# Optimization experiments

Measured on AMD Instinct MI355X. Metric: run time of the kernel, lower is better.

The kernel has to match this reference:

```python
import jax, jax.numpy as jnp
import numpy as np

N, E, D, H, G, C = 50000, 800000, 128, 128, 256, 10
BN_EPS = 1e-5

def _lin_init(key, fan_in, fan_out):
    k1, k2 = jax.random.split(key)
    bound = 1.0 / np.sqrt(fan_in)
    w = jax.random.uniform(k1, (fan_in, fan_out), jnp.float32, -bound, bound)
    b = jax.random.uniform(k2, (fan_out,), jnp.float32, -bound, bound)
    return w, b

def setup_inputs() -> dict:
    key = jax.random.key(0)
    ks = jax.random.split(key, 16)
    x = jax.random.normal(ks[0], (N, D), jnp.float32)
    edge_index = jax.random.randint(ks[1], (2, E), 0, N, jnp.int64)
    batch = jnp.sort(jax.random.randint(ks[2], (N,), 0, G, jnp.int64))
    inp = {"x": x, "edge_index": edge_index, "batch": batch}
    # per-layer GIN MLP params: Linear-ReLU-Linear-ReLU-BN
    dims = [(D, H), (H, H), (H, H)]
    for i, (din, dh) in enumerate(dims, start=1):
        wa, ba = _lin_init(ks[2 + 2 * i], din, dh)
        wb, bb = _lin_init(ks[3 + 2 * i], dh, dh)
        inp[f"w{i}a"], inp[f"b{i}a"] = wa, ba
        inp[f"w{i}b"], inp[f"b{i}b"] = wb, bb
        inp[f"g{i}"] = jnp.ones((dh,), jnp.float32)
        inp[f"bt{i}"] = jnp.zeros((dh,), jnp.float32)
    inp["eps"] = jnp.zeros((3,), jnp.float32)  # train_eps=True, init 0
    inp["lw1"], inp["lb1"] = _lin_init(ks[10], H, H)
    inp["lw2"], inp["lb2"] = _lin_init(ks[11], H, C)
    return inp

def _gin_layer(x, src, dst, eps_i, wa, ba, wb, bb, g, bt):
    # scatter-add neighbor aggregation: out[i] = sum_{j->i} x[j]
    agg = jax.ops.segment_sum(x[src], dst, num_segments=N)
    h = (1.0 + eps_i) * x + agg
    h = jax.nn.relu(h @ wa + ba)
    h = jax.nn.relu(h @ wb + bb)
    mu = h.mean(axis=0)
    var = ((h - mu) ** 2).mean(axis=0)  # biased var (torch BN normalization)
    return g * (h - mu) * jax.lax.rsqrt(var + BN_EPS) + bt

def reference(x, edge_index, batch, w1a, b1a, w1b, b1b, g1, bt1,
              w2a, b2a, w2b, b2b, g2, bt2, w3a, b3a, w3b, b3b, g3, bt3,
              eps, lw1, lb1, lw2, lb2):
    src, dst = edge_index[0], edge_index[1]
    h = _gin_layer(x, src, dst, eps[0], w1a, b1a, w1b, b1b, g1, bt1)
    h = _gin_layer(h, src, dst, eps[1], w2a, b2a, w2b, b2b, g2, bt2)
    h = _gin_layer(h, src, dst, eps[2], w3a, b3a, w3b, b3b, g3, bt3)
    # global mean pool over batch ids
    sums = jax.ops.segment_sum(h, batch, num_segments=G)
    cnt = jax.ops.segment_sum(jnp.ones((N,), h.dtype), batch, num_segments=G)
    pooled = sums / jnp.maximum(cnt, 1.0)[:, None]
    z = jax.nn.relu(pooled @ lw1 + lb1)
    # dropout omitted (eval / deterministic reference)
    z = z @ lw2 + lb2
    return jax.nn.log_softmax(z, axis=-1)
```

## Files before the change

### kernel.cpp

```cpp
#include <hip/hip_runtime.h>

#define N_NODES 50000
#define N_EDGES 800000
#define DIM 128
#define N_GRAPHS 256
#define N_CLS 10
#define BN_EPSV 1e-5f
#define CAP 64
#define RSIZE 6250
#define NBLK ((N_NODES + 63) / 64)

typedef __attribute__((ext_vector_type(8))) short short8;
typedef __attribute__((ext_vector_type(4))) float f32x4;

__device__ __forceinline__ float bf2f(short u) {
  return __uint_as_float(((unsigned)(unsigned short)u) << 16);
}
__device__ __forceinline__ unsigned short f2bf(float f) {
  unsigned u = __float_as_uint(f);
  unsigned r = (u + 0x7FFFu + ((u >> 16) & 1u)) >> 16;
  return (unsigned short)r;
}
__device__ __forceinline__ int swz(int row, int bytecol) {
  return row * 256 + (bytecol ^ ((row & 7) << 4));
}


__global__ void cvt_x_kernel(const float* __restrict__ x, ushort* __restrict__ xb) {
  int i = blockIdx.x * blockDim.x + threadIdx.x;
  int stride = gridDim.x * blockDim.x;
  const int tot = N_NODES * DIM / 4;
  for (; i < tot; i += stride) {
    float4 v = ((const float4*)x)[i];
    ushort4 o;
    o.x = f2bf(v.x); o.y = f2bf(v.y); o.z = f2bf(v.z); o.w = f2bf(v.w);
    ((ushort4*)xb)[i] = o;
  }
}

__global__ void cvt_w_kernel(const float* __restrict__ w0, const float* __restrict__ w1,
                             const float* __restrict__ w2, const float* __restrict__ w3,
                             const float* __restrict__ w4, const float* __restrict__ w5,
                             ushort* __restrict__ wt) {
  int m = blockIdx.x >> 6;
  const float* w = m == 0 ? w0 : m == 1 ? w1 : m == 2 ? w2 : m == 3 ? w3
                                                       : m == 4 ? w4 : w5;
  int idx = (blockIdx.x & 63) * 256 + threadIdx.x;
  int k = idx >> 7, n = idx & 127;
  wt[m * 16384 + n * 128 + k] = f2bf(w[idx]);
}


__global__ __launch_bounds__(256) void fill_kernel(
    const int* __restrict__ src, const int* __restrict__ dst,
    int* __restrict__ cnt, ushort* __restrict__ csr) {
  int cls = blockIdx.x & 7;
  int lo = cls * RSIZE;
  int hi = lo + RSIZE;
  int i = (blockIdx.x >> 3) * blockDim.x + threadIdx.x;
  int stride = (gridDim.x >> 3) * blockDim.x;
  for (; i < N_EDGES; i += stride) {
    int d = dst[i];
    if (d >= lo && d < hi) {
      int p = atomicAdd(&cnt[d], 1);
      if (p < CAP) csr[(size_t)d * CAP + p] = (ushort)src[i];
    }
  }
}


template <bool FIRST>
__global__ __launch_bounds__(256, 8) void gather_kernel(
    const ushort* __restrict__ xin, const int* __restrict__ cnt,
    const ushort* __restrict__ csr, const float* __restrict__ pstats,
    const float* __restrict__ pgamma, const float* __restrict__ pbeta,
    const float* __restrict__ epsp, int layer, ushort* __restrict__ agg) {
  int node = (blockIdx.x * blockDim.x + threadIdx.x) >> 6;
  if (node >= N_NODES) return;
  int l = threadIdx.x & 63;
  int li = l & 15, lg = l >> 4;
  float epv = 1.0f + epsp[layer];
  int deg = cnt[node];
  deg = deg < CAP ? deg : CAP;
  const ushort* nb = csr + (size_t)node * CAP;
  float av[8];
#pragma unroll
  for (int j = 0; j < 8; j++) av[j] = 0.f;
  if (lg == 0) {
    short8 sv = *(const short8*)(xin + (size_t)node * DIM + li * 8);
#pragma unroll
    for (int j = 0; j < 8; j++) av[j] = epv * bf2f(sv[j]);
  }
  int i = lg;
  for (; i + 12 < deg; i += 16) {
    int j0 = nb[i], j1 = nb[i + 4], j2 = nb[i + 8], j3 = nb[i + 12];
    short8 v0 = *(const short8*)(xin + (size_t)j0 * DIM + li * 8);
    short8 v1 = *(const short8*)(xin + (size_t)j1 * DIM + li * 8);
    short8 v2 = *(const short8*)(xin + (size_t)j2 * DIM + li * 8);
    short8 v3 = *(const short8*)(xin + (size_t)j3 * DIM + li * 8);
#pragma unroll
    for (int j = 0; j < 8; j++)
      av[j] += (bf2f(v0[j]) + bf2f(v1[j])) + (bf2f(v2[j]) + bf2f(v3[j]));
  }
  for (; i < deg; i += 4) {
    int j0 = nb[i];
    short8 v0 = *(const short8*)(xin + (size_t)j0 * DIM + li * 8);
#pragma unroll
    for (int j = 0; j < 8; j++) av[j] += bf2f(v0[j]);
  }
#pragma unroll
  for (int j = 0; j < 8; j++) {
    av[j] += __shfl_xor(av[j], 16, 64);
    av[j] += __shfl_xor(av[j], 32, 64);
  }
  if (lg == 0) {
    if (!FIRST) {
      const float invN = 1.0f / N_NODES;
      float co = epv + (float)deg;
#pragma unroll
      for (int j = 0; j < 8; j++) {
        int c = li * 8 + j;
        float mu = pstats[c] * invN;
        float var = fmaxf(pstats[DIM + c] * invN - mu * mu, 0.f);
        float sc = pgamma[c] * rsqrtf(var + BN_EPSV);
        float sh = pbeta[c] - mu * sc;
        av[j] = sc * av[j] + co * sh;
      }
    }
    short8 uv;
#pragma unroll
    for (int j = 0; j < 8; j++) uv[j] = (short)f2bf(av[j]);
    *(short8*)(agg + (size_t)node * DIM + li * 8) = uv;
  }
}


__global__ __launch_bounds__(512, 8) void mlp_kernel(
    const ushort* __restrict__ agg, const ushort* __restrict__ W1T,
    const float* __restrict__ b1, const ushort* __restrict__ W2T,
    const float* __restrict__ b2, ushort* __restrict__ out,
    float* __restrict__ bstat) {
  __shared__ __align__(16) ushort As[64 * DIM];
  __shared__ __align__(16) ushort H1[64 * DIM];
  __shared__ float sums[8 * DIM];
  __shared__ float sqs[8 * DIM];
  int tid = threadIdx.x;
  int w8 = tid >> 6;
  int wg = w8 >> 1;
  int ch = w8 & 1;
  int l = tid & 63, li = l & 15, lg = l >> 4;
  int row0 = blockIdx.x * 64;
  for (int t = tid; t < 1024; t += 512) {
    int row = t >> 4, chunk = t & 15;
    int grow = row0 + row;
    short8 v = {};
    if (grow < N_NODES) v = *(const short8*)(agg + (size_t)grow * DIM + chunk * 8);
    *(short8*)((char*)As + swz(row, chunk * 16)) = v;
  }
  __syncthreads();
  {
    f32x4 acc[4] = {};
    short8 af[4];
#pragma unroll
    for (int ks = 0; ks < 4; ks++)
      af[ks] = *(const short8*)((char*)As + swz(16 * wg + li, ks * 64 + lg * 16));
#pragma unroll
    for (int ct4 = 0; ct4 < 4; ct4++) {
      int ct = ch * 4 + ct4;
      const char* wp = (const char*)W1T + (ct * 16 + li) * 256 + lg * 16;
#pragma unroll
      for (int ks = 0; ks < 4; ks++) {
        short8 bf = *(const short8*)(wp + ks * 64);
        acc[ct4] = __builtin_amdgcn_mfma_f32_16x16x32_bf16(af[ks], bf, acc[ct4], 0, 0, 0);
      }
    }
#pragma unroll
    for (int ct4 = 0; ct4 < 4; ct4++) {
      int ct = ch * 4 + ct4;
      float bv = b1[ct * 16 + li];
#pragma unroll
      for (int r = 0; r < 4; r++) {
        int row = 16 * wg + lg * 4 + r;
        *(ushort*)((char*)H1 + swz(row, (ct * 16 + li) * 2)) =
            f2bf(fmaxf(acc[ct4][r] + bv, 0.f));
      }
    }
  }
  __syncthreads();
  float ss[4] = {0, 0, 0, 0}, sq[4] = {0, 0, 0, 0};
  {
    f32x4 acc[4] = {};
    short8 af[4];
#pragma unroll
    for (int ks = 0; ks < 4; ks++)
      af[ks] = *(const short8*)((char*)H1 + swz(16 * wg + li, ks * 64 + lg * 16));
#pragma unroll
    for (int ct4 = 0; ct4 < 4; ct4++) {
      int ct = ch * 4 + ct4;
      const char* wp = (const char*)W2T + (ct * 16 + li) * 256 + lg * 16;
#pragma unroll
      for (int ks = 0; ks < 4; ks++) {
        short8 bf = *(const short8*)(wp + ks * 64);
        acc[ct4] = __builtin_amdgcn_mfma_f32_16x16x32_bf16(af[ks], bf, acc[ct4], 0, 0, 0);
      }
    }
#pragma unroll
    for (int ct4 = 0; ct4 < 4; ct4++) {
      int ct = ch * 4 + ct4;
      float bv = b2[ct * 16 + li];
#pragma unroll
      for (int r = 0; r < 4; r++) {
        int row = 16 * wg + lg * 4 + r;
        float v = fmaxf(acc[ct4][r] + bv, 0.f);
        *(ushort*)((char*)As + swz(row, (ct * 16 + li) * 2)) = f2bf(v);
        float vm = (row0 + row < N_NODES) ? v : 0.f;
        ss[ct4] += vm;
        sq[ct4] += vm * vm;
      }
    }
  }
#pragma unroll
  for (int ct4 = 0; ct4 < 4; ct4++) {
    ss[ct4] += __shfl_xor(ss[ct4], 16, 64);
    ss[ct4] += __shfl_xor(ss[ct4], 32, 64);
    sq[ct4] += __shfl_xor(sq[ct4], 16, 64);
    sq[ct4] += __shfl_xor(sq[ct4], 32, 64);
  }
  if (l < 16) {
#pragma unroll
    for (int ct4 = 0; ct4 < 4; ct4++) {
      sums[w8 * DIM + (ch * 4 + ct4) * 16 + l] = ss[ct4];
      sqs[w8 * DIM + (ch * 4 + ct4) * 16 + l] = sq[ct4];
      sums[w8 * DIM + ((1 - ch) * 4 + ct4) * 16 + l] = 0.f;
      sqs[w8 * DIM + ((1 - ch) * 4 + ct4) * 16 + l] = 0.f;
    }
  }
  __syncthreads();
  for (int t = tid; t < 1024; t += 512) {
    int row = t >> 4, chunk = t & 15;
    int grow = row0 + row;
    if (grow < N_NODES) {
      short8 v = *(const short8*)((char*)As + swz(row, chunk * 16));
      *(short8*)(out + (size_t)grow * DIM + chunk * 8) = v;
    }
  }
  if (tid < DIM) {
    float t1 = 0.f, t2 = 0.f;
#pragma unroll
    for (int g = 0; g < 8; g++) {
      t1 += sums[g * DIM + tid];
      t2 += sqs[g * DIM + tid];
    }
    bstat[(size_t)blockIdx.x * DIM + tid] = t1;
    bstat[((size_t)NBLK + blockIdx.x) * DIM + tid] = t2;
  }
}


__global__ __launch_bounds__(64) void stats_reduce_kernel(
    const float* __restrict__ bstat, float* __restrict__ stats) {
  int c = blockIdx.x;
  int t = threadIdx.x;
  const float* src = bstat + (c < DIM ? 0 : (size_t)NBLK * DIM) + (c & (DIM - 1));
  float a = 0.f;
  for (int b = t; b < NBLK; b += 64) a += src[(size_t)b * DIM];
#pragma unroll
  for (int m = 32; m >= 1; m >>= 1) a += __shfl_xor(a, m, 64);
  if (t == 0) stats[c] = a;
}


__global__ void bounds_kernel(const int* __restrict__ batch, int* __restrict__ gstart) {
  int i = blockIdx.x * blockDim.x + threadIdx.x;
  if (i >= N_NODES) return;
  int b = batch[i];
  int prev = (i == 0) ? -1 : batch[i - 1];
  for (int g = prev + 1; g <= b; g++) gstart[g] = i;
  if (i == N_NODES - 1)
    for (int g = b + 1; g <= N_GRAPHS; g++) gstart[g] = N_NODES;
}


__global__ __launch_bounds__(128) void pool2_kernel(const ushort* __restrict__ h,
    const int* __restrict__ gstart, float* __restrict__ pool) {
  int g = blockIdx.x, t = threadIdx.x;
  int s = gstart[g], e = gstart[g + 1];
  float a0 = 0.f, a1 = 0.f, a2 = 0.f, a3 = 0.f;
  int i = s;
  for (; i + 3 < e; i += 4) {
    a0 += bf2f((short)h[(size_t)(i + 0) * DIM + t]);
    a1 += bf2f((short)h[(size_t)(i + 1) * DIM + t]);
    a2 += bf2f((short)h[(size_t)(i + 2) * DIM + t]);
    a3 += bf2f((short)h[(size_t)(i + 3) * DIM + t]);
  }
  for (; i < e; i++) a0 += bf2f((short)h[(size_t)i * DIM + t]);
  float cn = (float)(e - s);
  if (cn < 1.f) cn = 1.f;
  pool[g * DIM + t] = ((a0 + a1) + (a2 + a3)) / cn;
}


__global__ __launch_bounds__(128) void final_kernel(const float* __restrict__ pool,
    const float* __restrict__ stats3,
    const float* __restrict__ gamma3, const float* __restrict__ beta3,
    const float* __restrict__ lw1, const float* __restrict__ lb1,
    const float* __restrict__ lw2, const float* __restrict__ lb2,
    float* __restrict__ out) {
  int g = blockIdx.x, t = threadIdx.x;
  __shared__ float p[DIM];
  __shared__ float part[2];
  __shared__ float z2[N_CLS];
  const float invN = 1.0f / N_NODES;
  float mu = stats3[t] * invN;
  float var = fmaxf(stats3[DIM + t] * invN - mu * mu, 0.f);
  float sc = gamma3[t] * rsqrtf(var + BN_EPSV);
  float sh = beta3[t] - mu * sc;
  p[t] = sc * pool[g * DIM + t] + sh;
  __syncthreads();
  float acc = lb1[t];
  for (int k = 0; k < DIM; k++) acc += p[k] * lw1[k * DIM + t];
  acc = fmaxf(acc, 0.f);
  for (int c = 0; c < N_CLS; c++) {
    float v = acc * lw2[t * N_CLS + c];
#pragma unroll
    for (int m = 32; m >= 1; m >>= 1) v += __shfl_xor(v, m, 64);
    if ((t & 63) == 0) part[t >> 6] = v;
    __syncthreads();
    if (t == 0) z2[c] = part[0] + part[1] + lb2[c];
    __syncthreads();
  }
  if (t == 0) {
    float mx = -1e30f;
    for (int c = 0; c < N_CLS; c++) mx = fmaxf(mx, z2[c]);
    float sum = 0.f;
    for (int c = 0; c < N_CLS; c++) sum += expf(z2[c] - mx);
    float lse = mx + logf(sum);
    for (int c = 0; c < N_CLS; c++) out[g * N_CLS + c] = z2[c] - lse;
  }
}


extern "C" void kernel_launch(void* const* d_in, const int* in_sizes, int n_in,
                              void* d_out, int out_size, void* d_ws, size_t ws_size,
                              hipStream_t stream) {
  const float* x = (const float*)d_in[0];
  const int* edge = (const int*)d_in[1];
  const int* batch = (const int*)d_in[2];
  const float *w[3][2], *bv[3][2], *gam[3], *bet[3];
  int idx = 3;
  for (int l = 0; l < 3; l++) {
    w[l][0] = (const float*)d_in[idx++]; bv[l][0] = (const float*)d_in[idx++];
    w[l][1] = (const float*)d_in[idx++]; bv[l][1] = (const float*)d_in[idx++];
    gam[l] = (const float*)d_in[idx++];  bet[l] = (const float*)d_in[idx++];
  }
  const float* eps = (const float*)d_in[idx++];
  const float* lw1 = (const float*)d_in[idx++];
  const float* lb1 = (const float*)d_in[idx++];
  const float* lw2 = (const float*)d_in[idx++];
  const float* lb2 = (const float*)d_in[idx++];

  char* ws = (char*)d_ws;
  size_t off_b = 0;
  auto alloc = [&](size_t b) -> char* {
    char* p = ws + off_b;
    off_b += (b + 255) & ~(size_t)255;
    return p;
  };
  int* cnt = (int*)alloc((size_t)N_NODES * 4);
  ushort* csr = (ushort*)alloc((size_t)N_NODES * CAP * 2);
  ushort* P0 = (ushort*)alloc((size_t)N_NODES * DIM * 2);
  ushort* P1 = (ushort*)alloc((size_t)N_NODES * DIM * 2);
  ushort* P2 = (ushort*)alloc((size_t)N_NODES * DIM * 2);
  ushort* wt = (ushort*)alloc((size_t)6 * 16384 * 2);
  float* stats = (float*)alloc(3 * 2 * DIM * 4);
  float* pool = (float*)alloc((size_t)N_GRAPHS * DIM * 4);
  int* gstart = (int*)alloc((size_t)(N_GRAPHS + 1) * 4);
  float* bstat = (float*)alloc((size_t)2 * NBLK * DIM * 4);

  hipMemsetAsync(cnt, 0, (size_t)N_NODES * 4, stream);

  const int* srcp = edge;
  const int* dstp = edge + N_EDGES;
  cvt_x_kernel<<<2048, 256, 0, stream>>>(x, P0);
  cvt_w_kernel<<<384, 256, 0, stream>>>(w[0][0], w[0][1], w[1][0], w[1][1],
                                        w[2][0], w[2][1], wt);
  fill_kernel<<<2048, 256, 0, stream>>>(srcp, dstp, cnt, csr);
  bounds_kernel<<<(N_NODES + 255) / 256, 256, 0, stream>>>(batch, gstart);

  const int gblk = (N_NODES * 64 + 255) / 256;
  gather_kernel<true><<<gblk, 256, 0, stream>>>(
      P0, cnt, csr, nullptr, nullptr, nullptr, eps, 0, P1);
  mlp_kernel<<<NBLK, 512, 0, stream>>>(P1, wt + 0 * 16384, bv[0][0],
                                       wt + 1 * 16384, bv[0][1], P2, bstat);
  stats_reduce_kernel<<<256, 64, 0, stream>>>(bstat, stats);
  gather_kernel<false><<<gblk, 256, 0, stream>>>(
      P2, cnt, csr, stats, gam[0], bet[0], eps, 1, P0);
  mlp_kernel<<<NBLK, 512, 0, stream>>>(P0, wt + 2 * 16384, bv[1][0],
                                       wt + 3 * 16384, bv[1][1], P1, bstat);
  stats_reduce_kernel<<<256, 64, 0, stream>>>(bstat, stats + 2 * DIM);
  gather_kernel<false><<<gblk, 256, 0, stream>>>(
      P1, cnt, csr, stats + 2 * DIM, gam[1], bet[1], eps, 2, P2);
  mlp_kernel<<<NBLK, 512, 0, stream>>>(P2, wt + 4 * 16384, bv[2][0],
                                       wt + 5 * 16384, bv[2][1], P0, bstat);
  stats_reduce_kernel<<<256, 64, 0, stream>>>(bstat, stats + 4 * DIM);

  pool2_kernel<<<N_GRAPHS, 128, 0, stream>>>(P0, gstart, pool);
  final_kernel<<<N_GRAPHS, 128, 0, stream>>>(pool, stats + 4 * DIM,
                                             gam[2], bet[2], lw1, lb1, lw2, lb2,
                                             (float*)d_out);
}
```

Measured before the change: 321.2 us.

## Fuse neighbor gather into the MLP kernel, aggregating directly into shared memory

The separate gather kernel is merged into the per-layer MLP kernel. Each of the 8 waves in a 512-thread block now aggregates 8 nodes and writes the BN-adjusted, bf16-converted sums straight into the swizzled shared tile, replacing the global agg buffer round trip and one launch per layer. The trade-off is less parallelism during the latency-bound gather phase: each wave handles 8 nodes in sequence, and the MFMA phase cannot start until the whole block's gather is done. One ping-pong buffer is also freed.

Result: faster. 314.6 us (-2.0%).

```diff
diff --git a/kernel.cpp b/kernel.cpp
--- a/kernel.cpp
+++ b/kernel.cpp
@@ -70,94 +70,89 @@
 
 
 template <bool FIRST>
-__global__ __launch_bounds__(256, 8) void gather_kernel(
+__global__ __launch_bounds__(512, 8) void layer_kernel(
     const ushort* __restrict__ xin, const int* __restrict__ cnt,
     const ushort* __restrict__ csr, const float* __restrict__ pstats,
     const float* __restrict__ pgamma, const float* __restrict__ pbeta,
-    const float* __restrict__ epsp, int layer, ushort* __restrict__ agg) {
-  int node = (blockIdx.x * blockDim.x + threadIdx.x) >> 6;
-  if (node >= N_NODES) return;
-  int l = threadIdx.x & 63;
-  int li = l & 15, lg = l >> 4;
-  float epv = 1.0f + epsp[layer];
-  int deg = cnt[node];
-  deg = deg < CAP ? deg : CAP;
-  const ushort* nb = csr + (size_t)node * CAP;
-  float av[8];
-#pragma unroll
-  for (int j = 0; j < 8; j++) av[j] = 0.f;
-  if (lg == 0) {
-    short8 sv = *(const short8*)(xin + (size_t)node * DIM + li * 8);
-#pragma unroll
-    for (int j = 0; j < 8; j++) av[j] = epv * bf2f(sv[j]);
-  }
-  int i = lg;
-  for (; i + 12 < deg; i += 16) {
-    int j0 = nb[i], j1 = nb[i + 4], j2 = nb[i + 8], j3 = nb[i + 12];
-    short8 v0 = *(const short8*)(xin + (size_t)j0 * DIM + li * 8);
-    short8 v1 = *(const short8*)(xin + (size_t)j1 * DIM + li * 8);
-    short8 v2 = *(const short8*)(xin + (size_t)j2 * DIM + li * 8);
-    short8 v3 = *(const short8*)(xin + (size_t)j3 * DIM + li * 8);
-#pragma unroll
-    for (int j = 0; j < 8; j++)
-      av[j] += (bf2f(v0[j]) + bf2f(v1[j])) + (bf2f(v2[j]) + bf2f(v3[j]));
-  }
-  for (; i < deg; i += 4) {
-    int j0 = nb[i];
-    short8 v0 = *(const short8*)(xin + (size_t)j0 * DIM + li * 8);
-#pragma unroll
-    for (int j = 0; j < 8; j++) av[j] += bf2f(v0[j]);
-  }
-#pragma unroll
-  for (int j = 0; j < 8; j++) {
-    av[j] += __shfl_xor(av[j], 16, 64);
-    av[j] += __shfl_xor(av[j], 32, 64);
-  }
-  if (lg == 0) {
-    if (!FIRST) {
-      const float invN = 1.0f / N_NODES;
-      float co = epv + (float)deg;
-#pragma unroll
-      for (int j = 0; j < 8; j++) {
-        int c = li * 8 + j;
-        float mu = pstats[c] * invN;
-        float var = fmaxf(pstats[DIM + c] * invN - mu * mu, 0.f);
-        float sc = pgamma[c] * rsqrtf(var + BN_EPSV);
-        float sh = pbeta[c] - mu * sc;
-        av[j] = sc * av[j] + co * sh;
-      }
-    }
-    short8 uv;
-#pragma unroll
-    for (int j = 0; j < 8; j++) uv[j] = (short)f2bf(av[j]);
-    *(short8*)(agg + (size_t)node * DIM + li * 8) = uv;
-  }
-}
-
-
-__global__ __launch_bounds__(512, 8) void mlp_kernel(
-    const ushort* __restrict__ agg, const ushort* __restrict__ W1T,
-    const float* __restrict__ b1, const ushort* __restrict__ W2T,
-    const float* __restrict__ b2, ushort* __restrict__ out,
-    float* __restrict__ bstat) {
+    const float* __restrict__ epsp, int layer,
+    const ushort* __restrict__ W1T, const float* __restrict__ b1,
+    const ushort* __restrict__ W2T, const float* __restrict__ b2,
+    ushort* __restrict__ out, float* __restrict__ bstat) {
   __shared__ __align__(16) ushort As[64 * DIM];
   __shared__ __align__(16) ushort H1[64 * DIM];
   __shared__ float sums[8 * DIM];
   __shared__ float sqs[8 * DIM];
   int tid = threadIdx.x;
   int w8 = tid >> 6;
+  int l = tid & 63, li = l & 15, lg = l >> 4;
+  int row0 = blockIdx.x * 64;
+  float epv = 1.0f + epsp[layer];
+  float sc8[8], sh8[8];
+  if (!FIRST) {
+    const float invN = 1.0f / N_NODES;
+#pragma unroll
+    for (int j = 0; j < 8; j++) {
+      int c = li * 8 + j;
+      float mu = pstats[c] * invN;
+      float var = fmaxf(pstats[DIM + c] * invN - mu * mu, 0.f);
+      float sc = pgamma[c] * rsqrtf(var + BN_EPSV);
+      sc8[j] = sc;
+      sh8[j] = pbeta[c] - mu * sc;
+    }
+  }
+  for (int n = 0; n < 8; n++) {
+    int nl = w8 * 8 + n;
+    int node = row0 + nl;
+    float av[8];
+#pragma unroll
+    for (int j = 0; j < 8; j++) av[j] = 0.f;
+    if (node < N_NODES) {
+      int deg = cnt[node];
+      deg = deg < CAP ? deg : CAP;
+      const ushort* nb = csr + (size_t)node * CAP;
+      if (lg == 0) {
+        short8 sv = *(const short8*)(xin + (size_t)node * DIM + li * 8);
+#pragma unroll
+        for (int j = 0; j < 8; j++) av[j] = epv * bf2f(sv[j]);
+      }
+      int i = lg;
+      for (; i + 12 < deg; i += 16) {
+        int j0 = nb[i], j1 = nb[i + 4], j2 = nb[i + 8], j3 = nb[i + 12];
+        short8 v0 = *(const short8*)(xin + (size_t)j0 * DIM + li * 8);
+        short8 v1 = *(const short8*)(xin + (size_t)j1 * DIM + li * 8);
+        short8 v2 = *(const short8*)(xin + (size_t)j2 * DIM + li * 8);
+        short8 v3 = *(const short8*)(xin + (size_t)j3 * DIM + li * 8);
+#pragma unroll
+        for (int j = 0; j < 8; j++)
+          av[j] += (bf2f(v0[j]) + bf2f(v1[j])) + (bf2f(v2[j]) + bf2f(v3[j]));
+      }
+      for (; i < deg; i += 4) {
+        int j0 = nb[i];
+        short8 v0 = *(const short8*)(xin + (size_t)j0 * DIM + li * 8);
+#pragma unroll
+        for (int j = 0; j < 8; j++) av[j] += bf2f(v0[j]);
+      }
+#pragma unroll
+      for (int j = 0; j < 8; j++) {
+        av[j] += __shfl_xor(av[j], 16, 64);
+        av[j] += __shfl_xor(av[j], 32, 64);
+      }
+      if (!FIRST && lg == 0) {
+        float co = epv + (float)deg;
+#pragma unroll
+        for (int j = 0; j < 8; j++) av[j] = sc8[j] * av[j] + co * sh8[j];
+      }
+    }
+    if (lg == 0) {
+      short8 uv;
+#pragma unroll
+      for (int j = 0; j < 8; j++) uv[j] = (short)f2bf(av[j]);
+      *(short8*)((char*)As + swz(nl, li * 16)) = uv;
+    }
+  }
+  __syncthreads();
   int wg = w8 >> 1;
   int ch = w8 & 1;
-  int l = tid & 63, li = l & 15, lg = l >> 4;
-  int row0 = blockIdx.x * 64;
-  for (int t = tid; t < 1024; t += 512) {
-    int row = t >> 4, chunk = t & 15;
-    int grow = row0 + row;
-    short8 v = {};
-    if (grow < N_NODES) v = *(const short8*)(agg + (size_t)grow * DIM + chunk * 8);
-    *(short8*)((char*)As + swz(row, chunk * 16)) = v;
-  }
-  __syncthreads();
   {
     f32x4 acc[4] = {};
     short8 af[4];
@@ -370,7 +365,6 @@
   ushort* csr = (ushort*)alloc((size_t)N_NODES * CAP * 2);
   ushort* P0 = (ushort*)alloc((size_t)N_NODES * DIM * 2);
   ushort* P1 = (ushort*)alloc((size_t)N_NODES * DIM * 2);
-  ushort* P2 = (ushort*)alloc((size_t)N_NODES * DIM * 2);
   ushort* wt = (ushort*)alloc((size_t)6 * 16384 * 2);
   float* stats = (float*)alloc(3 * 2 * DIM * 4);
   float* pool = (float*)alloc((size_t)N_GRAPHS * DIM * 4);
@@ -387,24 +381,20 @@
   fill_kernel<<<2048, 256, 0, stream>>>(srcp, dstp, cnt, csr);
   bounds_kernel<<<(N_NODES + 255) / 256, 256, 0, stream>>>(batch, gstart);
 
-  const int gblk = (N_NODES * 64 + 255) / 256;
-  gather_kernel<true><<<gblk, 256, 0, stream>>>(
-      P0, cnt, csr, nullptr, nullptr, nullptr, eps, 0, P1);
-  mlp_kernel<<<NBLK, 512, 0, stream>>>(P1, wt + 0 * 16384, bv[0][0],
-                                       wt + 1 * 16384, bv[0][1], P2, bstat);
+  layer_kernel<true><<<NBLK, 512, 0, stream>>>(
+      P0, cnt, csr, nullptr, nullptr, nullptr, eps, 0,
+      wt + 0 * 16384, bv[0][0], wt + 1 * 16384, bv[0][1], P1, bstat);
   stats_reduce_kernel<<<256, 64, 0, stream>>>(bstat, stats);
-  gather_kernel<false><<<gblk, 256, 0, stream>>>(
-      P2, cnt, csr, stats, gam[0], bet[0], eps, 1, P0);
-  mlp_kernel<<<NBLK, 512, 0, stream>>>(P0, wt + 2 * 16384, bv[1][0],
-                                       wt + 3 * 16384, bv[1][1], P1, bstat);
+  layer_kernel<false><<<NBLK, 512, 0, stream>>>(
+      P1, cnt, csr, stats, gam[0], bet[0], eps, 1,
+      wt + 2 * 16384, bv[1][0], wt + 3 * 16384, bv[1][1], P0, bstat);
   stats_reduce_kernel<<<256, 64, 0, stream>>>(bstat, stats + 2 * DIM);
-  gather_kernel<false><<<gblk, 256, 0, stream>>>(
-      P1, cnt, csr, stats + 2 * DIM, gam[1], bet[1], eps, 2, P2);
-  mlp_kernel<<<NBLK, 512, 0, stream>>>(P2, wt + 4 * 16384, bv[2][0],
-                                       wt + 5 * 16384, bv[2][1], P0, bstat);
+  layer_kernel<false><<<NBLK, 512, 0, stream>>>(
+      P0, cnt, csr, stats + 2 * DIM, gam[1], bet[1], eps, 2,
+      wt + 4 * 16384, bv[2][0], wt + 5 * 16384, bv[2][1], P1, bstat);
   stats_reduce_kernel<<<256, 64, 0, stream>>>(bstat, stats + 4 * DIM);
 
-  pool2_kernel<<<N_GRAPHS, 128, 0, stream>>>(P0, gstart, pool);
+  pool2_kernel<<<N_GRAPHS, 128, 0, stream>>>(P1, gstart, pool);
   final_kernel<<<N_GRAPHS, 128, 0, stream>>>(pool, stats + 4 * DIM,
                                              gam[2], bet[2], lw1, lb1, lw2, lb2,
                                              (float*)d_out);
```
